# Kernel optimization log

Hardware: AMD Instinct MI355X
Metric: run time of the kernel (lower is better)

The kernel has to match this reference:

```python
import jax, jax.numpy as jnp
import numpy as np

B, S, D = 2, 2048, 1024
H, KS = 16, 64

def setup_inputs() -> dict:
    key = jax.random.key(0)
    k1, k2, k3, k4, k5 = jax.random.split(key, 5)
    return {
        "x": jax.random.normal(k1, (B, S, D), dtype=jnp.float32),
        "Wq": jax.random.normal(k2, (D, KS, H), dtype=jnp.float32) * 0.02,
        "Wk": jax.random.normal(k3, (D, KS, H), dtype=jnp.float32) * 0.02,
        "Wv": jax.random.normal(k4, (D, KS, H), dtype=jnp.float32) * 0.02,
        "kernel": jax.random.normal(k5, (H * KS, KS), dtype=jnp.float32) * 0.02,
    }

def reference(x, Wq, Wk, Wv, kernel):
    b, s, d = x.shape
    ks, h = Wq.shape[1], Wq.shape[2]
    # projections: heads-last layout [b, s, ks, h]
    q = jnp.einsum('bsd,dkh->bskh', x, Wq)
    k = jnp.einsum('bsd,dkh->bskh', x, Wk)
    v = jnp.einsum('bsd,dkh->bskh', x, Wv)
    # scores [b, i(query), l(key), h]
    scores = jnp.einsum('bikh,blkh->bilh', q, k) / jnp.sqrt(jnp.float32(ks))
    # strictly-upper-triangular (future) mask, as in the original:
    # band_part(ones,0,-1) - eye  ->  1 where l > i
    li = jnp.arange(s)
    mask = (li[None, :] > li[:, None]).astype(jnp.float32)  # [s, s]
    scores = scores - 1e8 * mask[None, :, :, None]
    weights = jax.nn.softmax(scores, axis=2)  # softmax over key axis l
    heads = jnp.einsum('bilh,blkh->bikh', weights, v)  # [b, s, ks, h]
    heads = heads.reshape(b, s, ks * h)  # row-major flatten of (ks, h), matching tf.reshape
    return heads @ kernel  # [b, s, ks]
```

## Files before the change

kernel.cpp:

```cpp
#include <hip/hip_runtime.h>
#include <hip/hip_bf16.h>

#define BB 2
#define SS 2048
#define DD 1024
#define HH 16
#define KSZ 64

typedef __attribute__((ext_vector_type(8))) short s16x8;
typedef __attribute__((ext_vector_type(4))) short s16x4;
typedef __attribute__((ext_vector_type(4))) float f32x4;
typedef __attribute__((ext_vector_type(8))) unsigned short u16x8;
typedef __attribute__((ext_vector_type(4))) unsigned short u16x4;
typedef __attribute__((ext_vector_type(2))) unsigned int u32x2;
typedef unsigned short u16;

__device__ __forceinline__ u16 bf16rne(float f) {
  unsigned int u = __float_as_uint(f);
  unsigned int r = (u + 0x7FFFu + ((u >> 16) & 1u)) >> 16;
  return (u16)r;
}

__device__ __forceinline__ unsigned int cvtpk_bf16(float lo, float hi) {
  unsigned int r;
  asm("v_cvt_pk_bf16_f32 %0, %1, %2" : "=v"(r) : "v"(lo), "v"(hi));
  return r;
}

#if __has_builtin(__builtin_amdgcn_mfma_f32_16x16x16_bf16)
__device__ __forceinline__ f32x4 mfma16(s16x4 a, s16x4 b, f32x4 c) {
  return __builtin_amdgcn_mfma_f32_16x16x16_bf16(a, b, c, 0, 0, 0);
}
#elif __has_builtin(__builtin_amdgcn_mfma_f32_16x16x16bf16_1k)
__device__ __forceinline__ f32x4 mfma16(s16x4 a, s16x4 b, f32x4 c) {
  return __builtin_amdgcn_mfma_f32_16x16x16bf16_1k(a, b, c, 0, 0, 0);
}
#else
__device__ __forceinline__ f32x4 mfma16(s16x4 a, s16x4 b, f32x4 c) {
  asm("s_nop 1\n\tv_mfma_f32_16x16x16_bf16 %0, %1, %2, %0"
      : "+v"(c) : "v"(a), "v"(b));
  return c;
}
#endif

__device__ __forceinline__ void lds_dma16(const u16* g, u16* l) {
  __builtin_amdgcn_global_load_lds(
      (const __attribute__((address_space(1))) unsigned int*)(const void*)g,
      (__attribute__((address_space(3))) unsigned int*)(void*)l, 16, 0, 0);
}

__global__ __launch_bounds__(256) void prep_all(
    const float* __restrict__ x, const float* __restrict__ Wq,
    const float* __restrict__ Wk, const float* __restrict__ Wv,
    const float* __restrict__ kern, u16* __restrict__ xb,
    u16* __restrict__ Wt, u16* __restrict__ BpT) {
  __shared__ float Ts[64][65];
  const int bid = blockIdx.x;
  const int tid = threadIdx.x;
  if (bid < 2048) {
    int idx = (bid * 256 + tid) * 8;
    float4 a = *(const float4*)(x + idx);
    float4 b = *(const float4*)(x + idx + 4);
    u16x8 v;
    v[0] = bf16rne(a.x); v[1] = bf16rne(a.y); v[2] = bf16rne(a.z); v[3] = bf16rne(a.w);
    v[4] = bf16rne(b.x); v[5] = bf16rne(b.y); v[6] = bf16rne(b.z); v[7] = bf16rne(b.w);
    *(u16x8*)(xb + idx) = v;
  } else if (bid < 2816) {
    const int bx = bid - 2048;
    const int p = bx >> 8, rem = bx & 255;
    const int d0 = (rem & 15) * 64, n0 = (rem >> 4) * 64;
    const float* W = (p == 0) ? Wq : (p == 1) ? Wk : Wv;
    u16* Wo = Wt + (size_t)p * DD * DD;
    #pragma unroll
    for (int i = 0; i < 4; ++i) {
      int f4 = tid + i * 256;
      int r = f4 >> 4, c4 = f4 & 15;
      float4 v = *(const float4*)(W + (size_t)(d0 + r) * DD + n0 + c4 * 4);
      Ts[r][c4 * 4 + 0] = v.x; Ts[r][c4 * 4 + 1] = v.y;
      Ts[r][c4 * 4 + 2] = v.z; Ts[r][c4 * 4 + 3] = v.w;
    }
    __syncthreads();
    #pragma unroll
    for (int i = 0; i < 4; ++i) {
      int ch = tid + i * 256;
      int n = ch >> 4, d4 = ch & 15;
      u16x4 o;
      #pragma unroll
      for (int j = 0; j < 4; ++j) o[j] = bf16rne(Ts[d4 * 4 + j][n]);
      *(u16x4*)(Wo + (size_t)(n0 + n) * DD + d0 + d4 * 4) = o;
    }
  } else {
    const int n = bid - 2816;
    const int k4 = tid * 4;
    u16x4 o;
    #pragma unroll
    for (int j = 0; j < 4; ++j) {
      int kp = k4 + j;
      int h = kp >> 6, k = kp & 63;
      o[j] = bf16rne(kern[(size_t)(k * HH + h) * KSZ + n]);
    }
    *(u16x4*)(BpT + (size_t)n * (HH * KSZ) + k4) = o;
  }
}

__global__ __launch_bounds__(512, 6) void proj_kernel(
    const u16* __restrict__ xb, const u16* __restrict__ Wt,
    u16* __restrict__ qkvT) {
  const int xcd = blockIdx.x & 7;
  const int idx = blockIdx.x >> 3;
  const int mt = (xcd >> 1) * 8 + (idx & 7);
  const int nt = (xcd & 1) * 4 + ((idx >> 3) & 3);
  const int p  = idx >> 5;
  const int m0 = mt * 128, n0 = nt * 128;
  const u16* W = Wt + (size_t)p * DD * DD;
  u16* outp = qkvT + (size_t)p * (BB * HH * SS * KSZ);

  __shared__ __align__(16) unsigned char raw[49152];
  u16* lds = (u16*)raw;
  u16* Cs  = (u16*)raw;

  const int tid = threadIdx.x;
  const int wave = tid >> 6, lane = tid & 63;
  const int g = lane >> 4, c = lane & 15;
  const int mbase = (wave & 1) * 64, nbase = (wave >> 1) * 32;

  const int lr = lane >> 2, lc = lane & 3;
  const int swz = (lc ^ ((lr >> 1) & 3)) * 8;
  const int rS = wave * 16;
  const u16* srcA = xb + (size_t)(m0 + rS + lr) * DD + swz;
  const u16* srcB = W  + (size_t)(n0 + rS + lr) * DD + swz;
  const int sl = rS * 32;

  f32x4 acc[4][2];
  #pragma unroll
  for (int i = 0; i < 4; ++i)
    #pragma unroll
    for (int j = 0; j < 2; ++j) acc[i][j] = {0.f, 0.f, 0.f, 0.f};

  {
    u16* A0 = lds;                u16* B0 = lds + 4096;
    u16* A1 = lds + 8192;         u16* B1 = lds + 8192 + 4096;
    lds_dma16(srcA, A0 + sl);       lds_dma16(srcB, B0 + sl);
    lds_dma16(srcA + 32, A1 + sl);  lds_dma16(srcB + 32, B1 + sl);
  }

  const int jsw = (c >> 1) & 3;
  int cr = 0;
  #pragma unroll 1
  for (int t = 0; t < 31; ++t) {
    asm volatile("s_waitcnt vmcnt(2)" ::: "memory");
    __builtin_amdgcn_s_barrier();
    __builtin_amdgcn_sched_barrier(0);
    if (t <= 29) {
      const int st = cr ? cr - 1 : 2;
      const int ko = (t + 2) * 32;
      u16* An = lds + st * 8192;
      u16* Bn = An + 4096;
      lds_dma16(srcA + ko, An + sl);  lds_dma16(srcB + ko, Bn + sl);
    }
    u16* Ac = lds + cr * 8192;
    u16* Bc = Ac + 4096;
    s16x8 af[4], bfr[2];
    #pragma unroll
    for (int mf = 0; mf < 4; ++mf)
      af[mf] = *(const s16x8*)&Ac[(mbase + mf * 16 + c) * 32 + ((g ^ jsw) * 8)];
    #pragma unroll
    for (int nf = 0; nf < 2; ++nf)
      bfr[nf] = *(const s16x8*)&Bc[(nbase + nf * 16 + c) * 32 + ((g ^ jsw) * 8)];
    #pragma unroll
    for (int mf = 0; mf < 4; ++mf)
      #pragma unroll
      for (int nf = 0; nf < 2; ++nf)
        acc[mf][nf] = __builtin_amdgcn_mfma_f32_16x16x32_bf16(
            af[mf], bfr[nf], acc[mf][nf], 0, 0, 0);
    cr = (cr >= 2) ? 0 : cr + 1;
  }
  asm volatile("s_waitcnt vmcnt(0)" ::: "memory");
  __builtin_amdgcn_s_barrier();
  __builtin_amdgcn_sched_barrier(0);
  {
    u16* Ac = lds + cr * 8192;
    u16* Bc = Ac + 4096;
    s16x8 af[4], bfr[2];
    #pragma unroll
    for (int mf = 0; mf < 4; ++mf)
      af[mf] = *(const s16x8*)&Ac[(mbase + mf * 16 + c) * 32 + ((g ^ jsw) * 8)];
    #pragma unroll
    for (int nf = 0; nf < 2; ++nf)
      bfr[nf] = *(const s16x8*)&Bc[(nbase + nf * 16 + c) * 32 + ((g ^ jsw) * 8)];
    #pragma unroll
    for (int mf = 0; mf < 4; ++mf)
      #pragma unroll
      for (int nf = 0; nf < 2; ++nf)
        acc[mf][nf] = __builtin_amdgcn_mfma_f32_16x16x32_bf16(
            af[mf], bfr[nf], acc[mf][nf], 0, 0, 0);
  }
  __syncthreads();

  const float cscale = (p == 0) ? 0.125f * 1.44269504f : 1.0f;
  #pragma unroll
  for (int mf = 0; mf < 4; ++mf)
    #pragma unroll
    for (int nf = 0; nf < 2; ++nf)
      #pragma unroll
      for (int r = 0; r < 4; ++r)
        Cs[(mbase + mf * 16 + g * 4 + r) * 136 + nbase + nf * 16 + c] =
            bf16rne(acc[mf][nf][r] * cscale);
  __syncthreads();
  const int b = m0 >> 11;
  if (p < 2) {
    int hh = tid >> 5, s5 = tid & 31;
    #pragma unroll
    for (int i = 0; i < 4; ++i) {
      int row = i * 32 + s5;
      int s = (m0 + row) & 2047;
      u16x8 v;
      #pragma unroll
      for (int kp = 0; kp < 8; ++kp) v[kp] = Cs[row * 136 + kp * 16 + hh];
      *(u16x8*)(outp + ((size_t)(b * HH + hh) * SS + s) * KSZ + (n0 >> 4)) = v;
    }
  } else {
    const int s0 = m0 & 2047;
    #pragma unroll
    for (int i = 0; i < 4; ++i) {
      int chunk = tid + i * 512;
      int colid = chunk >> 4;
      int hh = colid >> 3, kp = colid & 7;
      int s8 = chunk & 15;
      u16x8 v;
      #pragma unroll
      for (int j = 0; j < 8; ++j) v[j] = Cs[(s8 * 8 + j) * 136 + kp * 16 + hh];
      *(u16x8*)(outp + ((size_t)(b * HH + hh) * KSZ + (n0 >> 4) + kp) * SS +
                s0 + s8 * 8) = v;
    }
  }
}

__global__ __launch_bounds__(256, 4) void attn_kernel(
    const u16* __restrict__ qkvT, u16* __restrict__ headsB) {
  const int bid = blockIdx.x;
  const int hb = bid & 31;
  const int u  = bid >> 5;
  const int x  = u & 7, w = u >> 3;
  const int it = (w == 0) ? x : (w == 1) ? 15 - x : (w == 2) ? 16 + x : 31 - x;
  const int h = hb & 15, b = hb >> 4;
  const size_t plane = (size_t)(b * HH + h) * SS * KSZ;
  const size_t PSZ = (size_t)BB * HH * SS * KSZ;
  const u16* Qg = qkvT + plane;
  const u16* Kg = qkvT + PSZ + plane;
  const u16* Vg = qkvT + 2 * PSZ + plane;

  __shared__ u16 Ks[2][64 * 64];
  __shared__ u16 Vt[2][64 * 64];

  const int tid = threadIdx.x;
  const int lane = tid & 63;
  const int g = lane >> 4, c = lane & 15;
  const int wq0 = (tid >> 6) * 16;
  const int sr = tid >> 3, sc = tid & 7;
  const int soA = sr * 64 + ((sc ^ (sr & 7)) * 8);
  const int soB = soA + 32 * 64;

  s16x8 bq0 = *(const s16x8*)(Qg + (size_t)(it * 64 + wq0 + c) * KSZ + g * 8);
  s16x8 bq1 = *(const s16x8*)(Qg + (size_t)(it * 64 + wq0 + c) * KSZ + 32 + g * 8);

  u16x8 kr0 = *(const u16x8*)(Kg + (size_t)sr * KSZ + sc * 8);
  u16x8 kr1 = *(const u16x8*)(Kg + (size_t)(sr + 32) * KSZ + sc * 8);
  u16x8 vr0 = *(const u16x8*)(Vg + (size_t)sr * SS + sc * 8);
  u16x8 vr1 = *(const u16x8*)(Vg + (size_t)(sr + 32) * SS + sc * 8);
  *(u16x8*)&Ks[0][soA] = kr0; *(u16x8*)&Ks[0][soB] = kr1;
  *(u16x8*)&Vt[0][soA] = vr0; *(u16x8*)&Vt[0][soB] = vr1;
  kr0 = *(const u16x8*)(Kg + (size_t)(64 + sr) * KSZ + sc * 8);
  kr1 = *(const u16x8*)(Kg + (size_t)(64 + sr + 32) * KSZ + sc * 8);
  vr0 = *(const u16x8*)(Vg + (size_t)sr * SS + 64 + sc * 8);
  vr1 = *(const u16x8*)(Vg + (size_t)(sr + 32) * SS + 64 + sc * 8);
  __syncthreads();

  f32x4 o[4];
  #pragma unroll
  for (int mf = 0; mf < 4; ++mf) o[mf] = {0.f, 0.f, 0.f, 0.f};
  float l_i = 0.f;
  const int cswz = c & 7;
  const int qloc = wq0 + c;

  #pragma unroll 1
  for (int t = 0; t <= it; ++t) {
    const int buf = t & 1;
    if (t < it) {
      const int nb = buf ^ 1;
      *(u16x8*)&Ks[nb][soA] = kr0; *(u16x8*)&Ks[nb][soB] = kr1;
      *(u16x8*)&Vt[nb][soA] = vr0; *(u16x8*)&Vt[nb][soB] = vr1;
      if (t + 2 <= it) {
        const int kv2 = t + 2;
        kr0 = *(const u16x8*)(Kg + (size_t)(kv2 * 64 + sr) * KSZ + sc * 8);
        kr1 = *(const u16x8*)(Kg + (size_t)(kv2 * 64 + sr + 32) * KSZ + sc * 8);
        vr0 = *(const u16x8*)(Vg + (size_t)sr * SS + kv2 * 64 + sc * 8);
        vr1 = *(const u16x8*)(Vg + (size_t)(sr + 32) * SS + kv2 * 64 + sc * 8);
      }
    }
    f32x4 s[4];
    #pragma unroll
    for (int mf = 0; mf < 4; ++mf) s[mf] = {0.f, 0.f, 0.f, 0.f};
    __builtin_amdgcn_s_setprio(1);
    #pragma unroll
    for (int ks = 0; ks < 2; ++ks) {
      const s16x8 bq = ks ? bq1 : bq0;
      #pragma unroll
      for (int mf = 0; mf < 4; ++mf) {
        s16x8 ak = *(const s16x8*)&Ks[buf][(mf * 16 + c) * 64 +
                                          (((ks * 4 + g) ^ cswz) * 8)];
        s[mf] = __builtin_amdgcn_mfma_f32_16x16x32_bf16(ak, bq, s[mf], 0, 0, 0);
      }
    }
    __builtin_amdgcn_s_setprio(0);
    if (t == it) {
      #pragma unroll
      for (int mf = 0; mf < 4; ++mf)
        #pragma unroll
        for (int r = 0; r < 4; ++r)
          if (mf * 16 + g * 4 + r > qloc) s[mf][r] = -1e30f;
    }
    s16x4 bp[4];
    #pragma unroll
    for (int mf = 0; mf < 4; ++mf) {
      float p0 = __builtin_amdgcn_exp2f(s[mf][0]);
      float p1 = __builtin_amdgcn_exp2f(s[mf][1]);
      float p2 = __builtin_amdgcn_exp2f(s[mf][2]);
      float p3 = __builtin_amdgcn_exp2f(s[mf][3]);
      l_i += (p0 + p1) + (p2 + p3);
      u32x2 pk;
      pk[0] = cvtpk_bf16(p0, p1);
      pk[1] = cvtpk_bf16(p2, p3);
      bp[mf] = __builtin_bit_cast(s16x4, pk);
    }
    __builtin_amdgcn_s_setprio(1);
    #pragma unroll
    for (int mf = 0; mf < 4; ++mf) {
      #pragma unroll
      for (int kb = 0; kb < 4; ++kb) {
        s16x4 av = *(const s16x4*)&Vt[buf][(mf * 16 + c) * 64 +
                                           (((kb * 2 + (g >> 1)) ^ cswz) * 8) +
                                           (g & 1) * 4];
        o[mf] = mfma16(av, bp[kb], o[mf]);
      }
    }
    __builtin_amdgcn_s_setprio(0);
    __syncthreads();
  }
  l_i += __shfl_xor(l_i, 16);
  l_i += __shfl_xor(l_i, 32);
  const float inv = 1.0f / l_i;
  const int q = it * 64 + wq0 + c;
  #pragma unroll
  for (int mf = 0; mf < 4; ++mf) {
    u16x4 hv;
    #pragma unroll
    for (int r = 0; r < 4; ++r) hv[r] = bf16rne(o[mf][r] * inv);
    *(u16x4*)(headsB + plane + (size_t)q * KSZ + mf * 16 + g * 4) = hv;
  }
}

__global__ __launch_bounds__(256) void out_kernel(
    const u16* __restrict__ headsB, const u16* __restrict__ BpT,
    float* __restrict__ out) {
  const int m0 = blockIdx.x * 16;
  const int tid = threadIdx.x;
  const int wave = tid >> 6, lane = tid & 63;
  const int g = lane >> 4, c = lane & 15;

  const int m = m0 + c;
  const int b = m >> 11, s = m & 2047;

  f32x4 acc[4];
  #pragma unroll
  for (int nf = 0; nf < 4; ++nf) acc[nf] = {0.f, 0.f, 0.f, 0.f};

  #pragma unroll
  for (int it = 0; it < 8; ++it) {
    const int kb = wave * 256 + it * 32;
    const int hh = kb >> 6, kk = (kb & 63) + g * 8;
    s16x8 a = *(const s16x8*)(headsB +
        ((size_t)(b * HH + hh) * SS + s) * KSZ + kk);
    #pragma unroll
    for (int nf = 0; nf < 4; ++nf) {
      s16x8 bf = *(const s16x8*)(BpT +
          (size_t)(nf * 16 + c) * (HH * KSZ) + kb + g * 8);
      acc[nf] = __builtin_amdgcn_mfma_f32_16x16x32_bf16(a, bf, acc[nf], 0, 0, 0);
    }
  }

  __shared__ __align__(16) float red[4][64][16];
  #pragma unroll
  for (int nf = 0; nf < 4; ++nf)
    *(f32x4*)&red[wave][lane][nf * 4] = acc[nf];
  __syncthreads();

  const int mi = tid >> 4, n4 = (tid & 15) * 4;
  const int gg = mi >> 2, rr = mi & 3;
  float4 res;
  float* rp = &res.x;
  #pragma unroll
  for (int j = 0; j < 4; ++j) {
    int n = n4 + j;
    int cc = n & 15, nf = n >> 4;
    rp[j] = red[0][gg * 16 + cc][nf * 4 + rr] + red[1][gg * 16 + cc][nf * 4 + rr] +
            red[2][gg * 16 + cc][nf * 4 + rr] + red[3][gg * 16 + cc][nf * 4 + rr];
  }
  *(float4*)(out + (size_t)(m0 + mi) * KSZ + n4) = res;
}

extern "C" void kernel_launch(void* const* d_in, const int* in_sizes, int n_in,
                              void* d_out, int out_size, void* d_ws, size_t ws_size,
                              hipStream_t stream) {
  const float* x    = (const float*)d_in[0];
  const float* Wq   = (const float*)d_in[1];
  const float* Wk   = (const float*)d_in[2];
  const float* Wv   = (const float*)d_in[3];
  const float* kern = (const float*)d_in[4];
  float* out = (float*)d_out;

  u16* xb     = (u16*)d_ws;
  u16* Wt     = xb + (size_t)4096 * 1024;
  u16* qkvT   = Wt + (size_t)3 * 1024 * 1024;
  u16* headsB = qkvT + (size_t)3 * BB * HH * SS * KSZ;
  u16* BpT    = headsB + (size_t)BB * HH * SS * KSZ;

  prep_all<<<dim3(2880), 256, 0, stream>>>(x, Wq, Wk, Wv, kern, xb, Wt, BpT);
  proj_kernel<<<dim3(768), 512, 0, stream>>>(xb, Wt, qkvT);
  attn_kernel<<<dim3(1024), 256, 0, stream>>>(qkvT, headsB);
  out_kernel<<<dim3(256), 256, 0, stream>>>(headsB, BpT, out);
}
```

Measured before the change: 159.6 us.

## Enlarge attention query tile to 128 rows per block for K/V reuse

Each attention block now handles 128 query rows instead of 64, with each wave computing two 16-row query sub-tiles that share the same K and V fragments loaded from LDS. This halves the grid to 512 blocks, halves global and LDS K/V traffic per query, and gives more MFMA work per LDS read. In exchange it doubles accumulator registers, lowers the launch-bounds occupancy target, uses a coarser diagonal tile with more masked work, and has fewer blocks for load balancing.

```diff
diff --git a/kernel.cpp b/kernel.cpp
--- a/kernel.cpp
+++ b/kernel.cpp
@@ -236,13 +236,12 @@
   }
 }
 
-__global__ __launch_bounds__(256, 4) void attn_kernel(
+__global__ __launch_bounds__(256, 2) void attn_kernel(
     const u16* __restrict__ qkvT, u16* __restrict__ headsB) {
   const int bid = blockIdx.x;
   const int hb = bid & 31;
-  const int u  = bid >> 5;
-  const int x  = u & 7, w = u >> 3;
-  const int it = (w == 0) ? x : (w == 1) ? 15 - x : (w == 2) ? 16 + x : 31 - x;
+  const int q5 = bid >> 5;
+  const int qt = (q5 < 8) ? q5 : 23 - q5;
   const int h = hb & 15, b = hb >> 4;
   const size_t plane = (size_t)(b * HH + h) * SS * KSZ;
   const size_t PSZ = (size_t)BB * HH * SS * KSZ;
@@ -256,13 +255,20 @@
   const int tid = threadIdx.x;
   const int lane = tid & 63;
   const int g = lane >> 4, c = lane & 15;
-  const int wq0 = (tid >> 6) * 16;
+  const int wq0 = (tid >> 6) * 32;
   const int sr = tid >> 3, sc = tid & 7;
   const int soA = sr * 64 + ((sc ^ (sr & 7)) * 8);
   const int soB = soA + 32 * 64;
 
-  s16x8 bq0 = *(const s16x8*)(Qg + (size_t)(it * 64 + wq0 + c) * KSZ + g * 8);
-  s16x8 bq1 = *(const s16x8*)(Qg + (size_t)(it * 64 + wq0 + c) * KSZ + 32 + g * 8);
+  const int nt = 2 * qt + 2;
+
+  s16x8 bq[2][2];
+  #pragma unroll
+  for (int sq = 0; sq < 2; ++sq) {
+    const size_t qrow = (size_t)(qt * 128 + wq0 + sq * 16 + c) * KSZ;
+    bq[sq][0] = *(const s16x8*)(Qg + qrow + g * 8);
+    bq[sq][1] = *(const s16x8*)(Qg + qrow + 32 + g * 8);
+  }
 
   u16x8 kr0 = *(const u16x8*)(Kg + (size_t)sr * KSZ + sc * 8);
   u16x8 kr1 = *(const u16x8*)(Kg + (size_t)(sr + 32) * KSZ + sc * 8);
@@ -276,21 +282,22 @@
   vr1 = *(const u16x8*)(Vg + (size_t)(sr + 32) * SS + 64 + sc * 8);
   __syncthreads();
 
-  f32x4 o[4];
-  #pragma unroll
-  for (int mf = 0; mf < 4; ++mf) o[mf] = {0.f, 0.f, 0.f, 0.f};
-  float l_i = 0.f;
+  f32x4 o[2][4];
+  #pragma unroll
+  for (int sq = 0; sq < 2; ++sq)
+    #pragma unroll
+    for (int mf = 0; mf < 4; ++mf) o[sq][mf] = {0.f, 0.f, 0.f, 0.f};
+  float l_i[2] = {0.f, 0.f};
   const int cswz = c & 7;
-  const int qloc = wq0 + c;
 
   #pragma unroll 1
-  for (int t = 0; t <= it; ++t) {
+  for (int t = 0; t < nt; ++t) {
     const int buf = t & 1;
-    if (t < it) {
+    if (t + 1 < nt) {
       const int nb = buf ^ 1;
       *(u16x8*)&Ks[nb][soA] = kr0; *(u16x8*)&Ks[nb][soB] = kr1;
       *(u16x8*)&Vt[nb][soA] = vr0; *(u16x8*)&Vt[nb][soB] = vr1;
-      if (t + 2 <= it) {
+      if (t + 2 < nt) {
         const int kv2 = t + 2;
         kr0 = *(const u16x8*)(Kg + (size_t)(kv2 * 64 + sr) * KSZ + sc * 8);
         kr1 = *(const u16x8*)(Kg + (size_t)(kv2 * 64 + sr + 32) * KSZ + sc * 8);
@@ -298,40 +305,52 @@
         vr1 = *(const u16x8*)(Vg + (size_t)(sr + 32) * SS + kv2 * 64 + sc * 8);
       }
     }
-    f32x4 s[4];
-    #pragma unroll
-    for (int mf = 0; mf < 4; ++mf) s[mf] = {0.f, 0.f, 0.f, 0.f};
+    f32x4 s[2][4];
+    #pragma unroll
+    for (int sq = 0; sq < 2; ++sq)
+      #pragma unroll
+      for (int mf = 0; mf < 4; ++mf) s[sq][mf] = {0.f, 0.f, 0.f, 0.f};
     __builtin_amdgcn_s_setprio(1);
     #pragma unroll
     for (int ks = 0; ks < 2; ++ks) {
-      const s16x8 bq = ks ? bq1 : bq0;
       #pragma unroll
       for (int mf = 0; mf < 4; ++mf) {
         s16x8 ak = *(const s16x8*)&Ks[buf][(mf * 16 + c) * 64 +
                                           (((ks * 4 + g) ^ cswz) * 8)];
-        s[mf] = __builtin_amdgcn_mfma_f32_16x16x32_bf16(ak, bq, s[mf], 0, 0, 0);
+        s[0][mf] = __builtin_amdgcn_mfma_f32_16x16x32_bf16(ak, bq[0][ks],
+                                                           s[0][mf], 0, 0, 0);
+        s[1][mf] = __builtin_amdgcn_mfma_f32_16x16x32_bf16(ak, bq[1][ks],
+                                                           s[1][mf], 0, 0, 0);
       }
     }
     __builtin_amdgcn_s_setprio(0);
-    if (t == it) {
-      #pragma unroll
-      for (int mf = 0; mf < 4; ++mf)
+    if (t >= 2 * qt) {
+      const int rel = (t - 2 * qt) * 64;
+      #pragma unroll
+      for (int sq = 0; sq < 2; ++sq) {
+        const int qloc = wq0 + sq * 16 + c;
         #pragma unroll
-        for (int r = 0; r < 4; ++r)
-          if (mf * 16 + g * 4 + r > qloc) s[mf][r] = -1e30f;
-    }
-    s16x4 bp[4];
-    #pragma unroll
-    for (int mf = 0; mf < 4; ++mf) {
-      float p0 = __builtin_amdgcn_exp2f(s[mf][0]);
-      float p1 = __builtin_amdgcn_exp2f(s[mf][1]);
-      float p2 = __builtin_amdgcn_exp2f(s[mf][2]);
-      float p3 = __builtin_amdgcn_exp2f(s[mf][3]);
-      l_i += (p0 + p1) + (p2 + p3);
-      u32x2 pk;
-      pk[0] = cvtpk_bf16(p0, p1);
-      pk[1] = cvtpk_bf16(p2, p3);
-      bp[mf] = __builtin_bit_cast(s16x4, pk);
+        for (int mf = 0; mf < 4; ++mf)
+          #pragma unroll
+          for (int r = 0; r < 4; ++r)
+            if (rel + mf * 16 + g * 4 + r > qloc) s[sq][mf][r] = -1e30f;
+      }
+    }
+    s16x4 bp[2][4];
+    #pragma unroll
+    for (int sq = 0; sq < 2; ++sq) {
+      #pragma unroll
+      for (int mf = 0; mf < 4; ++mf) {
+        float p0 = __builtin_amdgcn_exp2f(s[sq][mf][0]);
+        float p1 = __builtin_amdgcn_exp2f(s[sq][mf][1]);
+        float p2 = __builtin_amdgcn_exp2f(s[sq][mf][2]);
+        float p3 = __builtin_amdgcn_exp2f(s[sq][mf][3]);
+        l_i[sq] += (p0 + p1) + (p2 + p3);
+        u32x2 pk;
+        pk[0] = cvtpk_bf16(p0, p1);
+        pk[1] = cvtpk_bf16(p2, p3);
+        bp[sq][mf] = __builtin_bit_cast(s16x4, pk);
+      }
     }
     __builtin_amdgcn_s_setprio(1);
     #pragma unroll
@@ -341,22 +360,27 @@
         s16x4 av = *(const s16x4*)&Vt[buf][(mf * 16 + c) * 64 +
                                            (((kb * 2 + (g >> 1)) ^ cswz) * 8) +
                                            (g & 1) * 4];
-        o[mf] = mfma16(av, bp[kb], o[mf]);
+        o[0][mf] = mfma16(av, bp[0][kb], o[0][mf]);
+        o[1][mf] = mfma16(av, bp[1][kb], o[1][mf]);
       }
     }
     __builtin_amdgcn_s_setprio(0);
     __syncthreads();
   }
-  l_i += __shfl_xor(l_i, 16);
-  l_i += __shfl_xor(l_i, 32);
-  const float inv = 1.0f / l_i;
-  const int q = it * 64 + wq0 + c;
-  #pragma unroll
-  for (int mf = 0; mf < 4; ++mf) {
-    u16x4 hv;
-    #pragma unroll
-    for (int r = 0; r < 4; ++r) hv[r] = bf16rne(o[mf][r] * inv);
-    *(u16x4*)(headsB + plane + (size_t)q * KSZ + mf * 16 + g * 4) = hv;
+  #pragma unroll
+  for (int sq = 0; sq < 2; ++sq) {
+    float l = l_i[sq];
+    l += __shfl_xor(l, 16);
+    l += __shfl_xor(l, 32);
+    const float inv = 1.0f / l;
+    const int q = qt * 128 + wq0 + sq * 16 + c;
+    #pragma unroll
+    for (int mf = 0; mf < 4; ++mf) {
+      u16x4 hv;
+      #pragma unroll
+      for (int r = 0; r < 4; ++r) hv[r] = bf16rne(o[sq][mf][r] * inv);
+      *(u16x4*)(headsB + plane + (size_t)q * KSZ + mf * 16 + g * 4) = hv;
+    }
   }
 }
 
@@ -427,6 +451,6 @@
 
   prep_all<<<dim3(2880), 256, 0, stream>>>(x, Wq, Wk, Wv, kern, xb, Wt, BpT);
   proj_kernel<<<dim3(768), 512, 0, stream>>>(xb, Wt, qkvT);
-  attn_kernel<<<dim3(1024), 256, 0, stream>>>(qkvT, headsB);
+  attn_kernel<<<dim3(512), 256, 0, stream>>>(qkvT, headsB);
   out_kernel<<<dim3(256), 256, 0, stream>>>(headsB, BpT, out);
 }
```

Result: no change. 157.0 us, median of 2 (-1.6%).
